# Optimization experiments

Hardware: AMD Instinct MI355X
Metric: run time of the kernel (lower is better)

Reference implementation:

```python
import jax, jax.numpy as jnp
import numpy as np

TEMP = 1.0

def setup_inputs() -> dict:
    key = jax.random.key(0)
    k1, k2, k3 = jax.random.split(key, 3)
    B, C, H, W = 8, 256, 64, 64
    h = jax.random.normal(k1, (B, C, H, W), dtype=jnp.float32)
    xs = jax.random.normal(k2, (B, C, H, W), dtype=jnp.float32)
    ys = jax.random.normal(k3, (B, C, H, W), dtype=jnp.float32)
    return {"h": h, "xs": xs, "ys": ys}

def reference(h, xs, ys):
    B, C, H, W = h.shape
    Bs, Cs, Hs, Ws = xs.shape
    hf = h.reshape(B, C, H * W)            # [B, C, N]   N = H*W
    xf = xs.reshape(Bs, Cs, Hs * Ws)       # [B, C, M]   M = Hs*Ws
    yf = ys.reshape(ys.shape[0], ys.shape[1], -1)  # [B, C, M]
    # attention[b, n, m] = sum_c h[b,c,n] * xs[b,c,m]
    attn = jnp.einsum('bcn,bcm->bnm', hf, xf)
    attn = jax.nn.softmax(attn / TEMP, axis=2)  # softmax over support positions m
    # xxs[b, c, n] = sum_m ys[b,c,m] * attn[b,n,m]
    xxs = jnp.einsum('bcm,bnm->bcn', yf, attn)
    return xxs.reshape(B, C, H, W)
```

## Files before the change

kernel.cpp:

```cpp
#include <hip/hip_runtime.h>
#include <stdint.h>

#define B_ 8
#define C_ 256
#define N_ 4096
#define M_ 4096
#define NT 128
#define MT 64
#define PP 72
#define L2E 1.44269504f

typedef _Float16 f16x8 __attribute__((ext_vector_type(8)));
typedef _Float16 f16x4 __attribute__((ext_vector_type(4)));
typedef float f32x4 __attribute__((ext_vector_type(4)));

__device__ __forceinline__ void async16(const _Float16* g, _Float16* l) {
    __builtin_amdgcn_global_load_lds(
        (const __attribute__((address_space(1))) void*)g,
        (__attribute__((address_space(3))) void*)l, 16, 0, 0);
}

__global__ __launch_bounds__(256) void kPre(const float* __restrict__ xs,
                                            const float* __restrict__ ys,
                                            _Float16* __restrict__ kt,
                                            _Float16* __restrict__ vb) {
    int bx = blockIdx.x;
    int t = threadIdx.x;
    if (bx < 2048) {
        __shared__ float tile[64][65];
        int b = bx >> 8, rem = bx & 255;
        int c0 = (rem >> 6) * 64, m0 = (rem & 63) * 64;
        int cl = t >> 4, m4 = (t & 15) * 4;
#pragma unroll
        for (int i = 0; i < 4; i++) {
            int c = c0 + cl + i * 16;
            const float4 v = *(const float4*)(xs + ((size_t)(b * C_ + c) * M_) + m0 + m4);
            tile[m4 + 0][cl + i * 16] = v.x;
            tile[m4 + 1][cl + i * 16] = v.y;
            tile[m4 + 2][cl + i * 16] = v.z;
            tile[m4 + 3][cl + i * 16] = v.w;
        }
        __syncthreads();
        int ml = t >> 4, c4 = (t & 15) * 4;
#pragma unroll
        for (int i = 0; i < 4; i++) {
            int m = m0 + ml + i * 16;
            f16x4 o;
            o[0] = (_Float16)tile[ml + i * 16][c4 + 0];
            o[1] = (_Float16)tile[ml + i * 16][c4 + 1];
            o[2] = (_Float16)tile[ml + i * 16][c4 + 2];
            o[3] = (_Float16)tile[ml + i * 16][c4 + 3];
            *(f16x4*)(kt + ((size_t)(b * M_ + m) * C_) + c0 + c4) = o;
        }
    } else {
        size_t i = ((size_t)(bx - 2048) * 256 + t) * 4;
        float4 v = *(const float4*)(ys + i);
        f16x4 o;
        o[0] = (_Float16)v.x; o[1] = (_Float16)v.y;
        o[2] = (_Float16)v.z; o[3] = (_Float16)v.w;
        *(f16x4*)(vb + i) = o;
    }
}

__global__ __launch_bounds__(512, 2) void kAttn(const float* __restrict__ h,
                                                const _Float16* __restrict__ kt,
                                                const _Float16* __restrict__ vb,
                                                float* __restrict__ out) {
    __shared__ _Float16 sK[2][MT * 256];
    __shared__ _Float16 sQ[NT * 256];
    __shared__ _Float16 sP[NT * PP];
    __shared__ float sAlpha[NT];
    __shared__ float sL[NT];
    __shared__ int sFlag[2];

    const int t = threadIdx.x;
    const int w = t >> 6, lane = t & 63, quad = lane >> 4, l15 = lane & 15;
    const int b = blockIdx.x & 7;
    const int n0 = (blockIdx.x >> 3) * NT;
    const int nb = w * 16;
    const int cb = w * 32;

    const _Float16* srcKb = kt + (size_t)b * M_ * C_;
    const _Float16* srcVb = vb + (size_t)b * C_ * M_;

    if (t == 0) { sFlag[0] = 0; sFlag[1] = 0; }

    {
        int cl = t >> 4;
        int n8 = (t & 15) * 8;
#pragma unroll
        for (int i = 0; i < 8; i++) {
            int c = i * 32 + cl;
#pragma unroll
            for (int half = 0; half < 2; half++) {
                const float4 v = *(const float4*)(h + ((size_t)(b * C_ + c) * N_) + n0 + n8 + half * 4);
                float xv[4] = {v.x, v.y, v.z, v.w};
#pragma unroll
                for (int j = 0; j < 4; j++) {
                    int row = n8 + half * 4 + j;
                    sQ[row * 256 + (((c >> 3) ^ (row & 31)) << 3) + (c & 7)] = (_Float16)xv[j];
                }
            }
        }
#pragma unroll
        for (int j = 0; j < 4; j++) {
            int row = w * 8 + j * 2 + (lane >> 5);
            int logi = (lane & 31) ^ (row & 31);
            async16(srcKb + (size_t)row * C_ + logi * 8, &sK[0][(w * 8 + j * 2) * 256]);
        }
    }
    asm volatile("s_waitcnt lgkmcnt(0)" ::: "memory");
    __builtin_amdgcn_s_barrier();

    f16x8 qf[8];
    {
        int qrow = nb + l15;
#pragma unroll
        for (int ks = 0; ks < 8; ks++)
            qf[ks] = *(const f16x8*)(&sQ[qrow * 256 + ((((ks << 2) + quad) ^ (qrow & 31)) << 3)]);
    }
    asm volatile("s_waitcnt lgkmcnt(0)" ::: "memory");

    f32x4 o[2][8];
#pragma unroll
    for (int i = 0; i < 2; i++)
#pragma unroll
        for (int j = 0; j < 8; j++)
            o[i][j] = (f32x4){0.f, 0.f, 0.f, 0.f};

    float mst = -3.0e38f, lp = 0.f;

    for (int it = 0; it < M_ / MT; it++) {
        const int cur = it & 1, nxt = cur ^ 1;
        const int m0i = it * MT;
        asm volatile("s_waitcnt vmcnt(0)" ::: "memory");
        __builtin_amdgcn_s_barrier();

        if (t == 0) sFlag[nxt] = 0;

        f16x8 vf[2][2];
#pragma unroll
        for (int ks = 0; ks < 2; ks++)
#pragma unroll
            for (int ct = 0; ct < 2; ct++) {
                int vrow = cb + ct * 16 + l15;
                vf[ks][ct] = *(const f16x8*)(srcVb + (size_t)vrow * M_ + m0i + ks * 32 + quad * 8);
            }
        __builtin_amdgcn_sched_barrier(0);

        if (it + 1 < M_ / MT) {
            const _Float16* srcK = srcKb + (size_t)(m0i + MT) * C_;
#pragma unroll
            for (int j = 0; j < 4; j++) {
                int row = w * 8 + j * 2 + (lane >> 5);
                int logi = (lane & 31) ^ (row & 31);
                async16(srcK + (size_t)row * C_ + logi * 8, &sK[nxt][(w * 8 + j * 2) * 256]);
            }
        }

        f32x4 s[4];
#pragma unroll
        for (int mt = 0; mt < 4; mt++) s[mt] = (f32x4){0.f, 0.f, 0.f, 0.f};
        __builtin_amdgcn_s_setprio(1);
#pragma unroll
        for (int ks = 0; ks < 8; ks++) {
#pragma unroll
            for (int mt = 0; mt < 4; mt++) {
                int krow = mt * 16 + l15;
                f16x8 bk = *(const f16x8*)(&sK[cur][krow * 256 + ((((ks << 2) + quad) ^ (krow & 31)) << 3)]);
                s[mt] = __builtin_amdgcn_mfma_f32_16x16x32_f16(bk, qf[ks], s[mt], 0, 0, 0);
            }
        }
        __builtin_amdgcn_s_setprio(0);

        float rowmax = fmaxf(fmaxf(fmaxf(s[0][0], s[0][1]), fmaxf(s[0][2], s[0][3])),
                             fmaxf(fmaxf(s[1][0], s[1][1]), fmaxf(s[1][2], s[1][3])));
        rowmax = fmaxf(rowmax, fmaxf(fmaxf(fmaxf(s[2][0], s[2][1]), fmaxf(s[2][2], s[2][3])),
                                     fmaxf(fmaxf(s[3][0], s[3][1]), fmaxf(s[3][2], s[3][3]))));
        rowmax = fmaxf(rowmax, __shfl_xor(rowmax, 16, 64));
        rowmax = fmaxf(rowmax, __shfl_xor(rowmax, 32, 64));
        float al = 1.0f;
        if (rowmax > mst) {
            al = exp2f((mst - rowmax) * L2E);
            mst = rowmax;
        }
        const float mb = mst * L2E;
        float psum = 0.f;
#pragma unroll
        for (int mt = 0; mt < 4; mt++)
#pragma unroll
            for (int r = 0; r < 4; r++) {
                float p = exp2f(s[mt][r] * L2E - mb);
                s[mt][r] = p;
                psum += p;
            }
        lp = lp * al + psum;
        if (quad == 0) {
            sAlpha[nb + l15] = al;
            if (al != 1.0f) atomicOr(&sFlag[cur], 1);
        }
#pragma unroll
        for (int mt = 0; mt < 4; mt++) {
            f16x4 pk;
            pk[0] = (_Float16)s[mt][0];
            pk[1] = (_Float16)s[mt][1];
            pk[2] = (_Float16)s[mt][2];
            pk[3] = (_Float16)s[mt][3];
            *(f16x4*)(&sP[(nb + l15) * PP + mt * 16 + quad * 4]) = pk;
        }

        asm volatile("s_waitcnt lgkmcnt(0)" ::: "memory");
        __builtin_amdgcn_s_barrier();

        if (sFlag[cur]) {
            float av[8];
#pragma unroll
            for (int nt = 0; nt < 8; nt++) av[nt] = sAlpha[nt * 16 + l15];
#pragma unroll
            for (int ct = 0; ct < 2; ct++)
#pragma unroll
                for (int nt = 0; nt < 8; nt++) {
                    o[ct][nt][0] *= av[nt];
                    o[ct][nt][1] *= av[nt];
                    o[ct][nt][2] *= av[nt];
                    o[ct][nt][3] *= av[nt];
                }
        }

        __builtin_amdgcn_s_setprio(1);
#pragma unroll
        for (int ks = 0; ks < 2; ks++) {
#pragma unroll
            for (int nt = 0; nt < 8; nt++) {
                f16x8 bp = *(const f16x8*)(sP + (nt * 16 + l15) * PP + ks * 32 + quad * 8);
#pragma unroll
                for (int ct = 0; ct < 2; ct++)
                    o[ct][nt] = __builtin_amdgcn_mfma_f32_16x16x32_f16(vf[ks][ct], bp, o[ct][nt], 0, 0, 0);
            }
        }
        __builtin_amdgcn_s_setprio(0);
    }

    lp += __shfl_xor(lp, 16, 64);
    lp += __shfl_xor(lp, 32, 64);
    if (quad == 0) sL[nb + l15] = lp;
    __syncthreads();
    float linv[8];
#pragma unroll
    for (int nt = 0; nt < 8; nt++) linv[nt] = 1.0f / sL[nt * 16 + l15];
#pragma unroll
    for (int ct = 0; ct < 2; ct++)
#pragma unroll
        for (int nt = 0; nt < 8; nt++)
#pragma unroll
            for (int r = 0; r < 4; r++) {
                int c = cb + ct * 16 + quad * 4 + r;
                out[((size_t)(b * C_ + c)) * N_ + n0 + nt * 16 + l15] = o[ct][nt][r] * linv[nt];
            }
}

extern "C" void kernel_launch(void* const* d_in, const int* in_sizes, int n_in,
                              void* d_out, int out_size, void* d_ws, size_t ws_size,
                              hipStream_t stream) {
    const float* h  = (const float*)d_in[0];
    const float* xs = (const float*)d_in[1];
    const float* ys = (const float*)d_in[2];
    float* out = (float*)d_out;

    _Float16* kt  = (_Float16*)d_ws;
    _Float16* vbb = kt + (size_t)B_ * M_ * C_;

    kPre<<<dim3(2048 + 8192), 256, 0, stream>>>(xs, ys, kt, vbb);
    kAttn<<<dim3(B_ * (N_ / NT)), 512, 0, stream>>>(h, kt, vbb, out);
}
```

Before: 372.7 us.

## Software-pipeline PV of previous tile with QK of current tile, triple-buffer K

```diff
diff --git a/kernel.cpp b/kernel.cpp
--- a/kernel.cpp
+++ b/kernel.cpp
@@ -7,7 +7,6 @@
 #define M_ 4096
 #define NT 128
 #define MT 64
-#define PP 72
 #define L2E 1.44269504f
 
 typedef _Float16 f16x8 __attribute__((ext_vector_type(8)));
@@ -66,28 +65,42 @@
                                                 const _Float16* __restrict__ kt,
                                                 const _Float16* __restrict__ vb,
                                                 float* __restrict__ out) {
-    __shared__ _Float16 sK[2][MT * 256];
-    __shared__ _Float16 sQ[NT * 256];
-    __shared__ _Float16 sP[NT * PP];
-    __shared__ float sAlpha[NT];
+    __shared__ _Float16 sK3[3][MT * 256];
+    __shared__ _Float16 sP[2][NT * 64];
+    __shared__ float sAlpha[2][NT];
     __shared__ float sL[NT];
-    __shared__ int sFlag[2];
+    __shared__ int sFlag[3];
 
     const int t = threadIdx.x;
     const int w = t >> 6, lane = t & 63, quad = lane >> 4, l15 = lane & 15;
     const int b = blockIdx.x & 7;
     const int n0 = (blockIdx.x >> 3) * NT;
     const int nb = w * 16;
-    const int cb = w * 32;
+    const int cb = (w & 3) * 64;
+    const int nh = (w >> 2) * 64;
 
     const _Float16* srcKb = kt + (size_t)b * M_ * C_;
     const _Float16* srcVb = vb + (size_t)b * C_ * M_;
 
-    if (t == 0) { sFlag[0] = 0; sFlag[1] = 0; }
+    if (t == 0) { sFlag[0] = 0; sFlag[1] = 0; sFlag[2] = 0; }
 
     {
+#pragma unroll
+        for (int j = 0; j < 4; j++) {
+            int row = w * 8 + j * 2 + (lane >> 5);
+            int logi = (lane & 31) ^ (row & 31);
+            async16(srcKb + (size_t)row * C_ + logi * 8, &sK3[0][(w * 8 + j * 2) * 256]);
+        }
+#pragma unroll
+        for (int j = 0; j < 4; j++) {
+            int row = w * 8 + j * 2 + (lane >> 5);
+            int logi = (lane & 31) ^ (row & 31);
+            async16(srcKb + (size_t)(MT + row) * C_ + logi * 8, &sK3[1][(w * 8 + j * 2) * 256]);
+        }
         int cl = t >> 4;
         int n8 = (t & 15) * 8;
+        _Float16* qdst = (n8 < 64) ? &sK3[2][0] : &sP[0][0];
+        int rbase = (n8 < 64) ? 0 : 64;
 #pragma unroll
         for (int i = 0; i < 8; i++) {
             int c = i * 32 + cl;
@@ -98,15 +111,9 @@
 #pragma unroll
                 for (int j = 0; j < 4; j++) {
                     int row = n8 + half * 4 + j;
-                    sQ[row * 256 + (((c >> 3) ^ (row & 31)) << 3) + (c & 7)] = (_Float16)xv[j];
-                }
-            }
-        }
-#pragma unroll
-        for (int j = 0; j < 4; j++) {
-            int row = w * 8 + j * 2 + (lane >> 5);
-            int logi = (lane & 31) ^ (row & 31);
-            async16(srcKb + (size_t)row * C_ + logi * 8, &sK[0][(w * 8 + j * 2) * 256]);
+                    qdst[(row - rbase) * 256 + (((c >> 3) ^ (row & 31)) << 3) + (c & 7)] = (_Float16)xv[j];
+                }
+            }
         }
     }
     asm volatile("s_waitcnt lgkmcnt(0)" ::: "memory");
@@ -115,68 +122,106 @@
     f16x8 qf[8];
     {
         int qrow = nb + l15;
+        const _Float16* qsrc = (qrow < 64) ? &sK3[2][0] : &sP[0][0];
+        int rloc = (nb < 64) ? qrow : qrow - 64;
 #pragma unroll
         for (int ks = 0; ks < 8; ks++)
-            qf[ks] = *(const f16x8*)(&sQ[qrow * 256 + ((((ks << 2) + quad) ^ (qrow & 31)) << 3)]);
-    }
-    asm volatile("s_waitcnt lgkmcnt(0)" ::: "memory");
-
-    f32x4 o[2][8];
-#pragma unroll
-    for (int i = 0; i < 2; i++)
-#pragma unroll
-        for (int j = 0; j < 8; j++)
+            qf[ks] = *(const f16x8*)(&qsrc[rloc * 256 + ((((ks << 2) + quad) ^ (qrow & 31)) << 3)]);
+    }
+    asm volatile("s_waitcnt lgkmcnt(0) vmcnt(4)" ::: "memory");
+    __builtin_amdgcn_s_barrier();
+
+    f32x4 o[4][4];
+#pragma unroll
+    for (int i = 0; i < 4; i++)
+#pragma unroll
+        for (int j = 0; j < 4; j++)
             o[i][j] = (f32x4){0.f, 0.f, 0.f, 0.f};
 
     float mst = -3.0e38f, lp = 0.f;
 
+    int fprev = 2, fcur = 0, fnext = 1;
+    int pp = 0;
+
     for (int it = 0; it < M_ / MT; it++) {
-        const int cur = it & 1, nxt = cur ^ 1;
-        const int m0i = it * MT;
-        asm volatile("s_waitcnt vmcnt(0)" ::: "memory");
-        __builtin_amdgcn_s_barrier();
-
-        if (t == 0) sFlag[nxt] = 0;
-
-        f16x8 vf[2][2];
-#pragma unroll
-        for (int ks = 0; ks < 2; ks++)
-#pragma unroll
-            for (int ct = 0; ct < 2; ct++) {
-                int vrow = cb + ct * 16 + l15;
-                vf[ks][ct] = *(const f16x8*)(srcVb + (size_t)vrow * M_ + m0i + ks * 32 + quad * 8);
-            }
+        if (t == 0) sFlag[fnext] = 0;
+
+        f16x8 vf[2][4];
+        if (it > 0) {
+            int m0p = (it - 1) * MT;
+#pragma unroll
+            for (int ks = 0; ks < 2; ks++)
+#pragma unroll
+                for (int ct = 0; ct < 4; ct++) {
+                    int vrow = cb + ct * 16 + l15;
+                    vf[ks][ct] = *(const f16x8*)(srcVb + (size_t)vrow * M_ + m0p + ks * 32 + quad * 8);
+                }
+        }
         __builtin_amdgcn_sched_barrier(0);
 
-        if (it + 1 < M_ / MT) {
-            const _Float16* srcK = srcKb + (size_t)(m0i + MT) * C_;
+        if (it < M_ / MT - 2) {
+            const _Float16* srcK = srcKb + (size_t)(it + 2) * MT * C_;
+            _Float16* dst = &sK3[fprev][0];
 #pragma unroll
             for (int j = 0; j < 4; j++) {
                 int row = w * 8 + j * 2 + (lane >> 5);
                 int logi = (lane & 31) ^ (row & 31);
-                async16(srcK + (size_t)row * C_ + logi * 8, &sK[nxt][(w * 8 + j * 2) * 256]);
-            }
-        }
-
-        f32x4 s[4];
-#pragma unroll
-        for (int mt = 0; mt < 4; mt++) s[mt] = (f32x4){0.f, 0.f, 0.f, 0.f};
+                async16(srcK + (size_t)row * C_ + logi * 8, dst + (w * 8 + j * 2) * 256);
+            }
+        }
+
+        if (it > 0 && sFlag[fprev]) {
+            float av[4];
+#pragma unroll
+            for (int nt = 0; nt < 4; nt++) av[nt] = sAlpha[pp ^ 1][nh + nt * 16 + l15];
+#pragma unroll
+            for (int ct = 0; ct < 4; ct++)
+#pragma unroll
+                for (int nt = 0; nt < 4; nt++) {
+                    o[ct][nt][0] *= av[nt];
+                    o[ct][nt][1] *= av[nt];
+                    o[ct][nt][2] *= av[nt];
+                    o[ct][nt][3] *= av[nt];
+                }
+        }
+
+        const _Float16* kcur = &sK3[fcur][0];
+        f32x4 s4[4];
+#pragma unroll
+        for (int mt = 0; mt < 4; mt++) s4[mt] = (f32x4){0.f, 0.f, 0.f, 0.f};
         __builtin_amdgcn_s_setprio(1);
 #pragma unroll
         for (int ks = 0; ks < 8; ks++) {
 #pragma unroll
             for (int mt = 0; mt < 4; mt++) {
                 int krow = mt * 16 + l15;
-                f16x8 bk = *(const f16x8*)(&sK[cur][krow * 256 + ((((ks << 2) + quad) ^ (krow & 31)) << 3)]);
-                s[mt] = __builtin_amdgcn_mfma_f32_16x16x32_f16(bk, qf[ks], s[mt], 0, 0, 0);
+                f16x8 bk = *(const f16x8*)(&kcur[krow * 256 + ((((ks << 2) + quad) ^ (krow & 31)) << 3)]);
+                s4[mt] = __builtin_amdgcn_mfma_f32_16x16x32_f16(bk, qf[ks], s4[mt], 0, 0, 0);
             }
         }
         __builtin_amdgcn_s_setprio(0);
 
-        float rowmax = fmaxf(fmaxf(fmaxf(s[0][0], s[0][1]), fmaxf(s[0][2], s[0][3])),
-                             fmaxf(fmaxf(s[1][0], s[1][1]), fmaxf(s[1][2], s[1][3])));
-        rowmax = fmaxf(rowmax, fmaxf(fmaxf(fmaxf(s[2][0], s[2][1]), fmaxf(s[2][2], s[2][3])),
-                                     fmaxf(fmaxf(s[3][0], s[3][1]), fmaxf(s[3][2], s[3][3]))));
+        if (it > 0) {
+            const _Float16* pprev = &sP[pp ^ 1][0];
+            __builtin_amdgcn_s_setprio(1);
+#pragma unroll
+            for (int ks = 0; ks < 2; ks++) {
+#pragma unroll
+                for (int nt = 0; nt < 4; nt++) {
+                    int prow = nh + nt * 16 + l15;
+                    f16x8 bp = *(const f16x8*)(&pprev[prow * 64 + ((((ks << 2) + quad) ^ (prow & 7)) << 3)]);
+#pragma unroll
+                    for (int ct = 0; ct < 4; ct++)
+                        o[ct][nt] = __builtin_amdgcn_mfma_f32_16x16x32_f16(vf[ks][ct], bp, o[ct][nt], 0, 0, 0);
+                }
+            }
+            __builtin_amdgcn_s_setprio(0);
+        }
+
+        float rowmax = fmaxf(fmaxf(fmaxf(s4[0][0], s4[0][1]), fmaxf(s4[0][2], s4[0][3])),
+                             fmaxf(fmaxf(s4[1][0], s4[1][1]), fmaxf(s4[1][2], s4[1][3])));
+        rowmax = fmaxf(rowmax, fmaxf(fmaxf(fmaxf(s4[2][0], s4[2][1]), fmaxf(s4[2][2], s4[2][3])),
+                                     fmaxf(fmaxf(s4[3][0], s4[3][1]), fmaxf(s4[3][2], s4[3][3]))));
         rowmax = fmaxf(rowmax, __shfl_xor(rowmax, 16, 64));
         rowmax = fmaxf(rowmax, __shfl_xor(rowmax, 32, 64));
         float al = 1.0f;
@@ -190,72 +235,92 @@
         for (int mt = 0; mt < 4; mt++)
 #pragma unroll
             for (int r = 0; r < 4; r++) {
-                float p = exp2f(s[mt][r] * L2E - mb);
-                s[mt][r] = p;
+                float p = exp2f(s4[mt][r] * L2E - mb);
+                s4[mt][r] = p;
                 psum += p;
             }
         lp = lp * al + psum;
         if (quad == 0) {
-            sAlpha[nb + l15] = al;
-            if (al != 1.0f) atomicOr(&sFlag[cur], 1);
-        }
-#pragma unroll
-        for (int mt = 0; mt < 4; mt++) {
-            f16x4 pk;
-            pk[0] = (_Float16)s[mt][0];
-            pk[1] = (_Float16)s[mt][1];
-            pk[2] = (_Float16)s[mt][2];
-            pk[3] = (_Float16)s[mt][3];
-            *(f16x4*)(&sP[(nb + l15) * PP + mt * 16 + quad * 4]) = pk;
+            sAlpha[pp][nb + l15] = al;
+            if (al != 1.0f) atomicOr(&sFlag[fcur], 1);
+        }
+
+        {
+            int prow = nb + l15;
+            _Float16* pdst = &sP[pp][0];
+#pragma unroll
+            for (int mt = 0; mt < 4; mt++) {
+                f16x4 pk;
+                pk[0] = (_Float16)s4[mt][0];
+                pk[1] = (_Float16)s4[mt][1];
+                pk[2] = (_Float16)s4[mt][2];
+                pk[3] = (_Float16)s4[mt][3];
+                *(f16x4*)(&pdst[prow * 64 + ((((mt << 1) + (quad >> 1)) ^ (prow & 7)) << 3) + ((quad & 1) << 2)]) = pk;
+            }
         }
 
         asm volatile("s_waitcnt lgkmcnt(0)" ::: "memory");
+        if (it < M_ / MT - 2) asm volatile("s_waitcnt vmcnt(4)" ::: "memory");
+        else                  asm volatile("s_waitcnt vmcnt(0)" ::: "memory");
         __builtin_amdgcn_s_barrier();
 
-        if (sFlag[cur]) {
-            float av[8];
-#pragma unroll
-            for (int nt = 0; nt < 8; nt++) av[nt] = sAlpha[nt * 16 + l15];
-#pragma unroll
-            for (int ct = 0; ct < 2; ct++)
-#pragma unroll
-                for (int nt = 0; nt < 8; nt++) {
+        int tmp = fprev; fprev = fcur; fcur = fnext; fnext = tmp;
+        pp ^= 1;
+    }
+
+    {
+        if (sFlag[fprev]) {
+            float av[4];
+#pragma unroll
+            for (int nt = 0; nt < 4; nt++) av[nt] = sAlpha[pp ^ 1][nh + nt * 16 + l15];
+#pragma unroll
+            for (int ct = 0; ct < 4; ct++)
+#pragma unroll
+                for (int nt = 0; nt < 4; nt++) {
                     o[ct][nt][0] *= av[nt];
                     o[ct][nt][1] *= av[nt];
                     o[ct][nt][2] *= av[nt];
                     o[ct][nt][3] *= av[nt];
                 }
         }
-
-        __builtin_amdgcn_s_setprio(1);
+        f16x8 vf[2][4];
+        int m0p = (M_ / MT - 1) * MT;
+#pragma unroll
+        for (int ks = 0; ks < 2; ks++)
+#pragma unroll
+            for (int ct = 0; ct < 4; ct++) {
+                int vrow = cb + ct * 16 + l15;
+                vf[ks][ct] = *(const f16x8*)(srcVb + (size_t)vrow * M_ + m0p + ks * 32 + quad * 8);
+            }
+        const _Float16* pprev = &sP[pp ^ 1][0];
 #pragma unroll
         for (int ks = 0; ks < 2; ks++) {
 #pragma unroll
-            for (int nt = 0; nt < 8; nt++) {
-                f16x8 bp = *(const f16x8*)(sP + (nt * 16 + l15) * PP + ks * 32 + quad * 8);
-#pragma unroll
-                for (int ct = 0; ct < 2; ct++)
+            for (int nt = 0; nt < 4; nt++) {
+                int prow = nh + nt * 16 + l15;
+                f16x8 bp = *(const f16x8*)(&pprev[prow * 64 + ((((ks << 2) + quad) ^ (prow & 7)) << 3)]);
+#pragma unroll
+                for (int ct = 0; ct < 4; ct++)
                     o[ct][nt] = __builtin_amdgcn_mfma_f32_16x16x32_f16(vf[ks][ct], bp, o[ct][nt], 0, 0, 0);
             }
         }
-        __builtin_amdgcn_s_setprio(0);
     }
 
     lp += __shfl_xor(lp, 16, 64);
     lp += __shfl_xor(lp, 32, 64);
     if (quad == 0) sL[nb + l15] = lp;
     __syncthreads();
-    float linv[8];
-#pragma unroll
-    for (int nt = 0; nt < 8; nt++) linv[nt] = 1.0f / sL[nt * 16 + l15];
-#pragma unroll
-    for (int ct = 0; ct < 2; ct++)
-#pragma unroll
-        for (int nt = 0; nt < 8; nt++)
+    float linv[4];
+#pragma unroll
+    for (int nt = 0; nt < 4; nt++) linv[nt] = 1.0f / sL[nh + nt * 16 + l15];
+#pragma unroll
+    for (int ct = 0; ct < 4; ct++)
+#pragma unroll
+        for (int nt = 0; nt < 4; nt++)
 #pragma unroll
             for (int r = 0; r < 4; r++) {
                 int c = cb + ct * 16 + quad * 4 + r;
-                out[((size_t)(b * C_ + c)) * N_ + n0 + nt * 16 + l15] = o[ct][nt][r] * linv[nt];
+                out[((size_t)(b * C_ + c)) * N_ + n0 + nh + nt * 16 + l15] = o[ct][nt][r] * linv[nt];
             }
 }
 
```

After: 404.7 us. +8.6%, slower.

## Switch attention to 32x32 MFMA with register-resident P via permlane swap

Applied to the files above, without the earlier changes.

```diff
diff --git a/kernel.cpp b/kernel.cpp
--- a/kernel.cpp
+++ b/kernel.cpp
@@ -7,17 +7,24 @@
 #define M_ 4096
 #define NT 128
 #define MT 64
-#define PP 72
 #define L2E 1.44269504f
 
 typedef _Float16 f16x8 __attribute__((ext_vector_type(8)));
 typedef _Float16 f16x4 __attribute__((ext_vector_type(4)));
-typedef float f32x4 __attribute__((ext_vector_type(4)));
+typedef _Float16 f16x2 __attribute__((ext_vector_type(2)));
+typedef float f32x16 __attribute__((ext_vector_type(16)));
+typedef unsigned int u32x4 __attribute__((ext_vector_type(4)));
 
 __device__ __forceinline__ void async16(const _Float16* g, _Float16* l) {
     __builtin_amdgcn_global_load_lds(
         (const __attribute__((address_space(1))) void*)g,
         (__attribute__((address_space(3))) void*)l, 16, 0, 0);
+}
+
+__device__ __forceinline__ void plswap(unsigned &a, unsigned &b) {
+    auto r = __builtin_amdgcn_permlane32_swap(a, b, false, false);
+    a = r[0];
+    b = r[1];
 }
 
 __global__ __launch_bounds__(256) void kPre(const float* __restrict__ xs,
@@ -67,196 +74,157 @@
                                                 const _Float16* __restrict__ vb,
                                                 float* __restrict__ out) {
     __shared__ _Float16 sK[2][MT * 256];
-    __shared__ _Float16 sQ[NT * 256];
-    __shared__ _Float16 sP[NT * PP];
-    __shared__ float sAlpha[NT];
-    __shared__ float sL[NT];
-    __shared__ int sFlag[2];
 
     const int t = threadIdx.x;
-    const int w = t >> 6, lane = t & 63, quad = lane >> 4, l15 = lane & 15;
+    const int w = t >> 6, lane = t & 63, hh = lane >> 5, l31 = lane & 31;
     const int b = blockIdx.x & 7;
     const int n0 = (blockIdx.x >> 3) * NT;
-    const int nb = w * 16;
-    const int cb = w * 32;
+    const int ns = w & 3, ch = w >> 2;
 
     const _Float16* srcKb = kt + (size_t)b * M_ * C_;
     const _Float16* srcVb = vb + (size_t)b * C_ * M_;
 
-    if (t == 0) { sFlag[0] = 0; sFlag[1] = 0; }
-
+#pragma unroll
+    for (int j = 0; j < 4; j++) {
+        int row = w * 8 + j * 2 + hh;
+        int logi = l31 ^ (row & 31);
+        async16(srcKb + (size_t)row * C_ + logi * 8, &sK[0][(w * 8 + j * 2) * 256]);
+    }
+
+    f16x8 qf[16];
     {
-        int cl = t >> 4;
-        int n8 = (t & 15) * 8;
-#pragma unroll
-        for (int i = 0; i < 8; i++) {
-            int c = i * 32 + cl;
-#pragma unroll
-            for (int half = 0; half < 2; half++) {
-                const float4 v = *(const float4*)(h + ((size_t)(b * C_ + c) * N_) + n0 + n8 + half * 4);
-                float xv[4] = {v.x, v.y, v.z, v.w};
-#pragma unroll
-                for (int j = 0; j < 4; j++) {
-                    int row = n8 + half * 4 + j;
-                    sQ[row * 256 + (((c >> 3) ^ (row & 31)) << 3) + (c & 7)] = (_Float16)xv[j];
-                }
-            }
-        }
-#pragma unroll
-        for (int j = 0; j < 4; j++) {
-            int row = w * 8 + j * 2 + (lane >> 5);
-            int logi = (lane & 31) ^ (row & 31);
-            async16(srcKb + (size_t)row * C_ + logi * 8, &sK[0][(w * 8 + j * 2) * 256]);
-        }
-    }
-    asm volatile("s_waitcnt lgkmcnt(0)" ::: "memory");
-    __builtin_amdgcn_s_barrier();
-
-    f16x8 qf[8];
-    {
-        int qrow = nb + l15;
-#pragma unroll
-        for (int ks = 0; ks < 8; ks++)
-            qf[ks] = *(const f16x8*)(&sQ[qrow * 256 + ((((ks << 2) + quad) ^ (qrow & 31)) << 3)]);
-    }
-    asm volatile("s_waitcnt lgkmcnt(0)" ::: "memory");
-
-    f32x4 o[2][8];
-#pragma unroll
-    for (int i = 0; i < 2; i++)
-#pragma unroll
-        for (int j = 0; j < 8; j++)
-            o[i][j] = (f32x4){0.f, 0.f, 0.f, 0.f};
+        const float* hq = h + (size_t)b * C_ * N_ + n0 + ns * 32 + l31;
+#pragma unroll
+        for (int ks = 0; ks < 16; ks++) {
+            f16x8 q;
+#pragma unroll
+            for (int i = 0; i < 8; i++)
+                q[i] = (_Float16)hq[(size_t)(ks * 16 + hh * 8 + i) * N_];
+            qf[ks] = q;
+        }
+    }
+
+    f32x16 o[4];
+#pragma unroll
+    for (int cq = 0; cq < 4; cq++)
+#pragma unroll
+        for (int r = 0; r < 16; r++) o[cq][r] = 0.f;
 
     float mst = -3.0e38f, lp = 0.f;
 
     for (int it = 0; it < M_ / MT; it++) {
         const int cur = it & 1, nxt = cur ^ 1;
         const int m0i = it * MT;
-        asm volatile("s_waitcnt vmcnt(0)" ::: "memory");
+        asm volatile("s_waitcnt vmcnt(0) lgkmcnt(0)" ::: "memory");
         __builtin_amdgcn_s_barrier();
 
-        if (t == 0) sFlag[nxt] = 0;
-
-        f16x8 vf[2][2];
-#pragma unroll
-        for (int ks = 0; ks < 2; ks++)
-#pragma unroll
-            for (int ct = 0; ct < 2; ct++) {
-                int vrow = cb + ct * 16 + l15;
-                vf[ks][ct] = *(const f16x8*)(srcVb + (size_t)vrow * M_ + m0i + ks * 32 + quad * 8);
-            }
+        f16x8 vf[4][4];
+#pragma unroll
+        for (int cq = 0; cq < 4; cq++)
+#pragma unroll
+            for (int ks = 0; ks < 4; ks++)
+                vf[cq][ks] = *(const f16x8*)(srcVb + (size_t)(ch * 128 + cq * 32 + l31) * M_
+                                             + m0i + ks * 16 + hh * 8);
         __builtin_amdgcn_sched_barrier(0);
 
         if (it + 1 < M_ / MT) {
             const _Float16* srcK = srcKb + (size_t)(m0i + MT) * C_;
 #pragma unroll
             for (int j = 0; j < 4; j++) {
-                int row = w * 8 + j * 2 + (lane >> 5);
-                int logi = (lane & 31) ^ (row & 31);
+                int row = w * 8 + j * 2 + hh;
+                int logi = l31 ^ (row & 31);
                 async16(srcK + (size_t)row * C_ + logi * 8, &sK[nxt][(w * 8 + j * 2) * 256]);
             }
         }
 
-        f32x4 s[4];
-#pragma unroll
-        for (int mt = 0; mt < 4; mt++) s[mt] = (f32x4){0.f, 0.f, 0.f, 0.f};
+        f32x16 sm[2];
+#pragma unroll
+        for (int mh = 0; mh < 2; mh++)
+#pragma unroll
+            for (int r = 0; r < 16; r++) sm[mh][r] = 0.f;
         __builtin_amdgcn_s_setprio(1);
 #pragma unroll
-        for (int ks = 0; ks < 8; ks++) {
-#pragma unroll
-            for (int mt = 0; mt < 4; mt++) {
-                int krow = mt * 16 + l15;
-                f16x8 bk = *(const f16x8*)(&sK[cur][krow * 256 + ((((ks << 2) + quad) ^ (krow & 31)) << 3)]);
-                s[mt] = __builtin_amdgcn_mfma_f32_16x16x32_f16(bk, qf[ks], s[mt], 0, 0, 0);
+        for (int ks = 0; ks < 16; ks++)
+#pragma unroll
+            for (int mh = 0; mh < 2; mh++) {
+                f16x8 bk = *(const f16x8*)(&sK[cur][(mh * 32 + l31) * 256
+                                                    + (((ks * 2 + hh) ^ l31) << 3)]);
+                sm[mh] = __builtin_amdgcn_mfma_f32_32x32x16_f16(bk, qf[ks], sm[mh], 0, 0, 0);
             }
-        }
         __builtin_amdgcn_s_setprio(0);
 
-        float rowmax = fmaxf(fmaxf(fmaxf(s[0][0], s[0][1]), fmaxf(s[0][2], s[0][3])),
-                             fmaxf(fmaxf(s[1][0], s[1][1]), fmaxf(s[1][2], s[1][3])));
-        rowmax = fmaxf(rowmax, fmaxf(fmaxf(fmaxf(s[2][0], s[2][1]), fmaxf(s[2][2], s[2][3])),
-                                     fmaxf(fmaxf(s[3][0], s[3][1]), fmaxf(s[3][2], s[3][3]))));
-        rowmax = fmaxf(rowmax, __shfl_xor(rowmax, 16, 64));
+        float tm[8];
+#pragma unroll
+        for (int j = 0; j < 8; j++)
+            tm[j] = fmaxf(fmaxf(sm[0][j], sm[0][j + 8]), fmaxf(sm[1][j], sm[1][j + 8]));
+#pragma unroll
+        for (int j = 0; j < 4; j++) tm[j] = fmaxf(tm[j], tm[j + 4]);
+        float rowmax = fmaxf(fmaxf(tm[0], tm[1]), fmaxf(tm[2], tm[3]));
         rowmax = fmaxf(rowmax, __shfl_xor(rowmax, 32, 64));
         float al = 1.0f;
-        if (rowmax > mst) {
-            al = exp2f((mst - rowmax) * L2E);
-            mst = rowmax;
-        }
+        if (rowmax > mst) { al = exp2f((mst - rowmax) * L2E); mst = rowmax; }
         const float mb = mst * L2E;
-        float psum = 0.f;
-#pragma unroll
-        for (int mt = 0; mt < 4; mt++)
-#pragma unroll
-            for (int r = 0; r < 4; r++) {
-                float p = exp2f(s[mt][r] * L2E - mb);
-                s[mt][r] = p;
-                psum += p;
+#pragma unroll
+        for (int mh = 0; mh < 2; mh++)
+#pragma unroll
+            for (int r = 0; r < 16; r++)
+                sm[mh][r] = exp2f(sm[mh][r] * L2E - mb);
+        float tp[8];
+#pragma unroll
+        for (int j = 0; j < 8; j++)
+            tp[j] = (sm[0][j] + sm[0][j + 8]) + (sm[1][j] + sm[1][j + 8]);
+#pragma unroll
+        for (int j = 0; j < 4; j++) tp[j] += tp[j + 4];
+        float ps = (tp[0] + tp[1]) + (tp[2] + tp[3]);
+        ps += __shfl_xor(ps, 32, 64);
+        lp = lp * al + ps;
+
+        if (al != 1.0f) {
+#pragma unroll
+            for (int cq = 0; cq < 4; cq++)
+#pragma unroll
+                for (int r = 0; r < 16; r++) o[cq][r] *= al;
+        }
+
+        f16x8 pfr[4];
+#pragma unroll
+        for (int mh = 0; mh < 2; mh++) {
+            unsigned pk[8];
+#pragma unroll
+            for (int j = 0; j < 8; j++) {
+                f16x2 pr;
+                pr[0] = (_Float16)sm[mh][2 * j];
+                pr[1] = (_Float16)sm[mh][2 * j + 1];
+                pk[j] = __builtin_bit_cast(unsigned, pr);
             }
-        lp = lp * al + psum;
-        if (quad == 0) {
-            sAlpha[nb + l15] = al;
-            if (al != 1.0f) atomicOr(&sFlag[cur], 1);
-        }
-#pragma unroll
-        for (int mt = 0; mt < 4; mt++) {
-            f16x4 pk;
-            pk[0] = (_Float16)s[mt][0];
-            pk[1] = (_Float16)s[mt][1];
-            pk[2] = (_Float16)s[mt][2];
-            pk[3] = (_Float16)s[mt][3];
-            *(f16x4*)(&sP[(nb + l15) * PP + mt * 16 + quad * 4]) = pk;
-        }
-
-        asm volatile("s_waitcnt lgkmcnt(0)" ::: "memory");
-        __builtin_amdgcn_s_barrier();
-
-        if (sFlag[cur]) {
-            float av[8];
-#pragma unroll
-            for (int nt = 0; nt < 8; nt++) av[nt] = sAlpha[nt * 16 + l15];
-#pragma unroll
-            for (int ct = 0; ct < 2; ct++)
-#pragma unroll
-                for (int nt = 0; nt < 8; nt++) {
-                    o[ct][nt][0] *= av[nt];
-                    o[ct][nt][1] *= av[nt];
-                    o[ct][nt][2] *= av[nt];
-                    o[ct][nt][3] *= av[nt];
-                }
+            plswap(pk[0], pk[2]);
+            plswap(pk[1], pk[3]);
+            plswap(pk[4], pk[6]);
+            plswap(pk[5], pk[7]);
+            u32x4 t0, t1;
+            t0[0] = pk[0]; t0[1] = pk[1]; t0[2] = pk[2]; t0[3] = pk[3];
+            t1[0] = pk[4]; t1[1] = pk[5]; t1[2] = pk[6]; t1[3] = pk[7];
+            pfr[2 * mh]     = __builtin_bit_cast(f16x8, t0);
+            pfr[2 * mh + 1] = __builtin_bit_cast(f16x8, t1);
         }
 
         __builtin_amdgcn_s_setprio(1);
 #pragma unroll
-        for (int ks = 0; ks < 2; ks++) {
-#pragma unroll
-            for (int nt = 0; nt < 8; nt++) {
-                f16x8 bp = *(const f16x8*)(sP + (nt * 16 + l15) * PP + ks * 32 + quad * 8);
-#pragma unroll
-                for (int ct = 0; ct < 2; ct++)
-                    o[ct][nt] = __builtin_amdgcn_mfma_f32_16x16x32_f16(vf[ks][ct], bp, o[ct][nt], 0, 0, 0);
-            }
-        }
+        for (int ks = 0; ks < 4; ks++)
+#pragma unroll
+            for (int cq = 0; cq < 4; cq++)
+                o[cq] = __builtin_amdgcn_mfma_f32_32x32x16_f16(vf[cq][ks], pfr[ks], o[cq], 0, 0, 0);
         __builtin_amdgcn_s_setprio(0);
     }
 
-    lp += __shfl_xor(lp, 16, 64);
-    lp += __shfl_xor(lp, 32, 64);
-    if (quad == 0) sL[nb + l15] = lp;
-    __syncthreads();
-    float linv[8];
-#pragma unroll
-    for (int nt = 0; nt < 8; nt++) linv[nt] = 1.0f / sL[nt * 16 + l15];
-#pragma unroll
-    for (int ct = 0; ct < 2; ct++)
-#pragma unroll
-        for (int nt = 0; nt < 8; nt++)
-#pragma unroll
-            for (int r = 0; r < 4; r++) {
-                int c = cb + ct * 16 + quad * 4 + r;
-                out[((size_t)(b * C_ + c)) * N_ + n0 + nt * 16 + l15] = o[ct][nt][r] * linv[nt];
-            }
+    const float linv = 1.0f / lp;
+#pragma unroll
+    for (int cq = 0; cq < 4; cq++)
+#pragma unroll
+        for (int r = 0; r < 16; r++) {
+            int c = ch * 128 + cq * 32 + (r & 3) + 8 * (r >> 2) + 4 * hh;
+            out[((size_t)(b * C_ + c)) * N_ + n0 + ns * 32 + l31] = o[cq][r] * linv;
+        }
 }
 
 extern "C" void kernel_launch(void* const* d_in, const int* in_sizes, int n_in,
```

Result: slower. 660.8 us (+77.3%).
